# Performance work log

Measured on AMD Instinct MI355X. Metric: run time of the kernel, lower is better.

## Reference

```python
import jax, jax.numpy as jnp
import numpy as np
from jax import lax

VOCAB = 50000; EMB = 128; HID = 256; NL = 9; B = 128; T = 512; H = HID // 2; PAD = 0


def setup_inputs() -> dict:
    key = jax.random.key(0)
    ks = jax.random.split(key, 16)
    p = lambda k, s: jax.random.normal(k, s, jnp.float32) * 0.05
    return {
        "chars": jax.random.randint(ks[0], (B, T), 1, VOCAB),  # in [1, VOCAB) so mask fully on
        "labels": jax.random.randint(ks[1], (B, T), 0, NL),
        "emb": p(ks[2], (VOCAB, EMB)),
        "W_ih_f": p(ks[3], (4 * H, EMB)), "W_hh_f": p(ks[4], (4 * H, H)),
        "b_ih_f": p(ks[5], (4 * H,)), "b_hh_f": p(ks[6], (4 * H,)),
        "W_ih_b": p(ks[7], (4 * H, EMB)), "W_hh_b": p(ks[8], (4 * H, H)),
        "b_ih_b": p(ks[9], (4 * H,)), "b_hh_b": p(ks[10], (4 * H,)),
        "W_out": p(ks[11], (NL, HID)), "b_out": p(ks[12], (NL,)),
        "start_trans": p(ks[13], (NL,)), "end_trans": p(ks[14], (NL,)),
        "trans": p(ks[15], (NL, NL)),
    }


def _lstm(x, Wih, Whh, bih, bhh, reverse):
    # x: (B, T, D); PyTorch gate order i, f, g, o
    bsz = x.shape[0]
    h0 = jnp.zeros((bsz, H), x.dtype)
    c0 = jnp.zeros((bsz, H), x.dtype)
    b = bih + bhh

    def step(carry, xt):
        h, c = carry
        g = xt @ Wih.T + h @ Whh.T + b  # (B, 4H)
        i, f, gg, o = jnp.split(g, 4, axis=-1)
        c = jax.nn.sigmoid(f) * c + jax.nn.sigmoid(i) * jnp.tanh(gg)
        h = jax.nn.sigmoid(o) * jnp.tanh(c)
        return (h, c), h

    _, hs = lax.scan(step, (h0, c0), jnp.swapaxes(x, 0, 1), reverse=reverse)
    return jnp.swapaxes(hs, 0, 1)  # (B, T, H)


def _crf_nll(emissions, labels, mask, start, end, trans):
    # torchcrf linear-chain CRF log-likelihood, reduction='sum'
    maskf = mask.astype(emissions.dtype)
    emit = jnp.take_along_axis(emissions, labels[..., None], 2)[..., 0]  # (B, T)
    score = start[labels[:, 0]] + (emit * maskf).sum(1)
    score = score + (trans[labels[:, :-1], labels[:, 1:]] * maskf[:, 1:]).sum(1)
    last_idx = mask.sum(1).astype(jnp.int32) - 1
    last_tags = jnp.take_along_axis(labels, last_idx[:, None], 1)[:, 0]
    score = score + end[last_tags]

    # forward algorithm (log partition) as a scan over time
    alpha0 = start[None, :] + emissions[:, 0]  # (B, L)

    def step(alpha, inp):
        e_t, m_t = inp  # (B, L), (B,)
        nxt = jax.nn.logsumexp(alpha[:, :, None] + trans[None, :, :], axis=1) + e_t
        return jnp.where(m_t[:, None], nxt, alpha), None

    alpha, _ = lax.scan(step, alpha0,
                        (jnp.swapaxes(emissions, 0, 1)[1:], jnp.swapaxes(mask, 0, 1)[1:]))
    logZ = jax.nn.logsumexp(alpha + end[None, :], axis=-1)
    return -(score - logZ).sum()


def reference(chars, labels, emb, W_ih_f, W_hh_f, b_ih_f, b_hh_f,
              W_ih_b, W_hh_b, b_ih_b, b_hh_b, W_out, b_out,
              start_trans, end_trans, trans):
    x = emb[chars]  # (B, T, EMB)
    hf = _lstm(x, W_ih_f, W_hh_f, b_ih_f, b_hh_f, False)
    hb = _lstm(x, W_ih_b, W_hh_b, b_ih_b, b_hh_b, True)
    h = jnp.concatenate([hf, hb], axis=-1)  # (B, T, HID)
    emissions = h @ W_out.T + b_out  # dropout is identity in eval mode
    mask = chars != PAD
    return _crf_nll(emissions, labels, mask, start_trans, end_trans, trans)
```

## Files before the change

### kernel.cpp

```cpp
#include <hip/hip_runtime.h>

#define B_   128
#define T_   512
#define EMB_ 128
#define H_   128
#define NL_  9
#define MT_  65536

typedef __attribute__((ext_vector_type(8))) short short8v;
typedef __attribute__((ext_vector_type(4))) float float4v;

__device__ inline unsigned short f2bf(float f){
  unsigned u = __float_as_uint(f);
  u += 0x7FFFu + ((u >> 16) & 1u);
  return (unsigned short)(u >> 16);
}
__device__ inline float bf2f(unsigned short s){
  return __uint_as_float(((unsigned)s) << 16);
}

#define LOG2E 1.44269504f
__device__ inline float vexp2(float x){ float r; asm("v_exp_f32 %0, %1" : "=v"(r) : "v"(x)); return r; }
__device__ inline float vrcp (float x){ float r; asm("v_rcp_f32 %0, %1" : "=v"(r) : "v"(x)); return r; }

__device__ inline float lstm_cell(float pi, float pf, float pg, float po, float& c){
  float ei = vexp2(-LOG2E * pi);
  float ef = vexp2(-LOG2E * pf);
  float eg = vexp2( 2.f * LOG2E * pg);
  float eo = vexp2(-LOG2E * po);
  float R1 = vrcp((1.f + ei) * (1.f + eg));
  float ig = (eg - 1.f) * R1;
  float F  = vrcp(1.f + ef);
  c = fmaf(F, c, ig);
  float ec = vexp2(2.f * LOG2E * c);
  float R2 = vrcp((1.f + eo) * (1.f + ec));
  return (ec - 1.f) * R2;
}

__device__ inline void bar(){
  __builtin_amdgcn_sched_barrier(0);
  asm volatile("s_waitcnt lgkmcnt(0)" ::: "memory");
  __builtin_amdgcn_sched_barrier(0);
  __builtin_amdgcn_s_barrier();
  __builtin_amdgcn_sched_barrier(0);
}

__global__ void k0_prep(const float* __restrict__ Wihf, const float* __restrict__ Whhf,
                        const float* __restrict__ bihf, const float* __restrict__ bhhf,
                        const float* __restrict__ Wihb, const float* __restrict__ Whhb,
                        const float* __restrict__ bihb, const float* __restrict__ bhhb,
                        unsigned short* __restrict__ Wih2, unsigned short* __restrict__ Whh2,
                        float* __restrict__ biasc){
  int blk = blockIdx.x;
  int dir = blk >> 9;
  int nd  = blk & 511;
  int k   = threadIdx.x;
  int j = nd >> 2, g = nd & 3;
  int orig = g * 128 + j;
  const float* Wih = dir ? Wihb : Wihf;
  const float* Whh = dir ? Whhb : Whhf;
  Wih2[((long)(dir * 512 + nd)) * 128 + k] = f2bf(Wih[orig * EMB_ + k]);
  Whh2[((long)(dir * 512 + nd)) * 128 + k] = f2bf(Whh[orig * H_ + k]);
  if (k == 0){
    const float* bi = dir ? bihb : bihf;
    const float* bh = dir ? bhhb : bhhf;
    biasc[dir * 512 + nd] = bi[orig] + bh[orig];
  }
}

__global__ void k1_embed(const int* __restrict__ chars, const float* __restrict__ emb,
                         unsigned short* __restrict__ x){
  int i = blockIdx.x * blockDim.x + threadIdx.x;
  int m = i >> 5, q = i & 31;
  int c = chars[m];
  const float4* e4 = (const float4*)(emb + (long)c * EMB_);
  float4 v = e4[q];
  ushort4 o;
  o.x = f2bf(v.x); o.y = f2bf(v.y); o.z = f2bf(v.z); o.w = f2bf(v.w);
  *(ushort4*)(x + (long)m * EMB_ + q * 4) = o;
}

#define CST 130
__global__ __launch_bounds__(256) void k2_gemm(const unsigned short* __restrict__ x,
                                               const unsigned short* __restrict__ Wih2,
                                               const float* __restrict__ biasc,
                                               unsigned short* __restrict__ G){
  __shared__ unsigned short gsm[64 * CST];
  int w = threadIdx.x >> 6, lane = threadIdx.x & 63;
  int r = lane & 15, kb = (lane >> 4) * 8;
  long arow = (long)(blockIdx.x * 64 + w * 16 + r);
  short8v a[4];
  #pragma unroll
  for (int kf = 0; kf < 4; kf++)
    a[kf] = *(const short8v*)(x + arow * EMB_ + kf * 32 + kb);
  int ncol0 = blockIdx.y * 128;
  float4v acc[8];
  #pragma unroll
  for (int nf = 0; nf < 8; nf++){
    float4v z = {0.f, 0.f, 0.f, 0.f};
    acc[nf] = z;
    int wrow = ncol0 + nf * 16 + r;
    #pragma unroll
    for (int kf = 0; kf < 4; kf++){
      short8v bfrag = *(const short8v*)(Wih2 + (long)wrow * 128 + kf * 32 + kb);
      acc[nf] = __builtin_amdgcn_mfma_f32_16x16x32_bf16(a[kf], bfrag, acc[nf], 0, 0, 0);
    }
  }
  int rloc0 = w * 16 + (lane >> 4) * 4;
  #pragma unroll
  for (int nf = 0; nf < 8; nf++){
    int col = ncol0 + nf * 16 + r;
    float bia = biasc[col];
    #pragma unroll
    for (int reg = 0; reg < 4; reg++)
      gsm[(rloc0 + reg) * CST + nf * 16 + r] = f2bf(acc[nf][reg] + bia);
  }
  __syncthreads();
  #pragma unroll
  for (int it = 0; it < 4; it++){
    int u = it * 256 + threadIdx.x;
    int row = u >> 4, cu = u & 15;
    short8v v = *(const short8v*)&gsm[row * CST + cu * 8];
    *(short8v*)(G + (long)(blockIdx.x * 64 + row) * 1024 + ncol0 + cu * 8) = v;
  }
}

#define HBST 136
__global__ __launch_bounds__(1024, 1) void k3_scan4(
    const unsigned short* __restrict__ G,
    const unsigned short* __restrict__ Whh2,
    unsigned short* __restrict__ hs)
{
  const int blk = blockIdx.x;
  const int dir = blk >> 3;
  const int b0  = (blk & 7) * 16;
  const int tid = threadIdx.x;
  const int w   = tid >> 6;
  const int l   = tid & 63;
  const int r   = l & 15;
  const int q   = l >> 4;

  __shared__ unsigned short hR[8][16 * HBST];

  short8v Wf[2][4];
  #pragma unroll
  for (int t = 0; t < 2; t++){
    const unsigned short* wp = Whh2 + ((long)(dir * 512 + 32 * w + 16 * t + r)) * 128 + q * 8;
    #pragma unroll
    for (int kf = 0; kf < 4; kf++)
      Wf[t][kf] = *(const short8v*)(wp + kf * 32);
  }
  #pragma unroll
  for (int t = 0; t < 2; t++)
    #pragma unroll
    for (int kf = 0; kf < 4; kf++)
      asm volatile("" : "+v"(Wf[t][kf]));

  for (int i = tid; i < 16 * HBST; i += 1024) hR[7][i] = 0;

  float cc0 = 0.f, cc1 = 0.f;
  const int j0 = 8 * w + q;
  const int j1 = j0 + 4;
  const int fii = tid >> 8, fmm = (tid >> 4) & 15, fj8 = tid & 15;

  const long gstep = dir ? -1024L : 1024L;
  const unsigned short* gbase = G + ((long)(b0 + r) * T_ + (dir ? T_ - 1 : 0)) * 1024
                                  + dir * 512 + 32 * w + 4 * q;

#define ISSUEX(D0A, D0B, D1A, D1B, S) do{                          \
    const unsigned short* p_ = gbase + (long)(S) * gstep;          \
    D0A = *(const ushort4*)(p_);                                   \
    D0B = *(const ushort4*)(p_ + 16);                              \
    D1A = *(const ushort4*)(p_ + gstep);                           \
    D1B = *(const ushort4*)(p_ + gstep + 16);                      \
  }while(0)

#define STEPX(S, GA, GB) do{                                       \
    const int slot_r = ((S) + 7) & 7, slot_w = (S) & 7;            \
    const unsigned short* hrow = &hR[slot_r][r * HBST + q * 8];    \
    short8v hf0 = *(const short8v*)(hrow);                         \
    short8v hf1 = *(const short8v*)(hrow + 32);                    \
    short8v hf2 = *(const short8v*)(hrow + 64);                    \
    short8v hf3 = *(const short8v*)(hrow + 96);                    \
    float4v acc0 = {bf2f((GA).x), bf2f((GA).y), bf2f((GA).z), bf2f((GA).w)}; \
    float4v acc1 = {bf2f((GB).x), bf2f((GB).y), bf2f((GB).z), bf2f((GB).w)}; \
    acc0 = __builtin_amdgcn_mfma_f32_16x16x32_bf16(Wf[0][0], hf0, acc0, 0, 0, 0); \
    acc0 = __builtin_amdgcn_mfma_f32_16x16x32_bf16(Wf[0][1], hf1, acc0, 0, 0, 0); \
    acc0 = __builtin_amdgcn_mfma_f32_16x16x32_bf16(Wf[0][2], hf2, acc0, 0, 0, 0); \
    acc0 = __builtin_amdgcn_mfma_f32_16x16x32_bf16(Wf[0][3], hf3, acc0, 0, 0, 0); \
    acc1 = __builtin_amdgcn_mfma_f32_16x16x32_bf16(Wf[1][0], hf0, acc1, 0, 0, 0); \
    acc1 = __builtin_amdgcn_mfma_f32_16x16x32_bf16(Wf[1][1], hf1, acc1, 0, 0, 0); \
    acc1 = __builtin_amdgcn_mfma_f32_16x16x32_bf16(Wf[1][2], hf2, acc1, 0, 0, 0); \
    acc1 = __builtin_amdgcn_mfma_f32_16x16x32_bf16(Wf[1][3], hf3, acc1, 0, 0, 0); \
    float hv0 = lstm_cell(acc0[0], acc0[1], acc0[2], acc0[3], cc0);\
    float hv1 = lstm_cell(acc1[0], acc1[1], acc1[2], acc1[3], cc1);\
    unsigned pk_;                                                  \
    asm("v_cvt_pk_bf16_f32 %0, %1, %2" : "=v"(pk_) : "v"(hv0), "v"(hv1)); \
    unsigned short* wr = &hR[slot_w][r * HBST];                    \
    wr[j0] = (unsigned short)(pk_ & 0xffffu);                      \
    wr[j1] = (unsigned short)(pk_ >> 16);                          \
    bar();                                                         \
  }while(0)

#define FLUSHX(S4) do{                                             \
    int sg_ = (S4) - 4 + fii;                                      \
    int tg_ = dir ? (T_ - 1 - sg_) : sg_;                          \
    short8v v_ = *(const short8v*)&hR[sg_ & 7][fmm * HBST + fj8 * 8]; \
    *(short8v*)(hs + ((long)dir * MT_ + (long)(b0 + fmm) * T_ + tg_) * H_ + fj8 * 8) = v_; \
  }while(0)

  ushort4 A0a, A0b, A1a, A1b, B0a, B0b, B1a, B1b;
  ISSUEX(A0a, A0b, A1a, A1b, 0);
  bar();

  for (int s4 = 0; s4 < T_; s4 += 4){
    if (s4 > 0) FLUSHX(s4);
    ISSUEX(B0a, B0b, B1a, B1b, s4 + 2);
    STEPX(s4 + 0, A0a, A0b);
    STEPX(s4 + 1, A1a, A1b);
    if (s4 + 4 < T_) ISSUEX(A0a, A0b, A1a, A1b, s4 + 4);
    STEPX(s4 + 2, B0a, B0b);
    STEPX(s4 + 3, B1a, B1b);
  }
  FLUSHX(T_);

#undef ISSUEX
#undef STEPX
#undef FLUSHX
}

#define HSTR 264
__global__ __launch_bounds__(512) void k4_emis(const unsigned short* __restrict__ hs,
                                               const float* __restrict__ Wout,
                                               const float* __restrict__ bout,
                                               float* __restrict__ em){
  __shared__ float hcat[64 * HSTR];
  __shared__ float wo[NL_ * 256];
  int tid = threadIdx.x;
  int m0 = blockIdx.x * 64;
  const unsigned short* hf = hs;
  const unsigned short* hb = hs + (long)MT_ * H_;
  #pragma unroll
  for (int it = 0; it < 8; it++){
    int flat = it * 2048 + tid * 4;
    int r = flat >> 8, u = flat & 255;
    const unsigned short* src = (u < 128) ? (hf + (long)(m0 + r) * H_ + u)
                                          : (hb + (long)(m0 + r) * H_ + (u - 128));
    ushort4 v = *(const ushort4*)src;
    hcat[r * HSTR + u]     = bf2f(v.x);
    hcat[r * HSTR + u + 1] = bf2f(v.y);
    hcat[r * HSTR + u + 2] = bf2f(v.z);
    hcat[r * HSTR + u + 3] = bf2f(v.w);
  }
  for (int f = tid; f < NL_ * 256; f += 512) wo[f] = Wout[f];
  __syncthreads();
  #pragma unroll
  for (int half = 0; half < 2; half++){
    int idx = half * 512 + tid;
    if (idx < 64 * NL_){
      int r = idx / NL_, lbl = idx % NL_;
      float acc = bout[lbl];
      #pragma unroll 8
      for (int u = 0; u < 256; u++)
        acc = fmaf(hcat[r * HSTR + u], wo[lbl * 256 + u], acc);
      em[(long)(m0 + r) * NL_ + lbl] = acc;
    }
  }
}

__global__ void k5_crf(const float* __restrict__ em, const int* __restrict__ chars,
                       const int* __restrict__ labels, const float* __restrict__ startv,
                       const float* __restrict__ endv, const float* __restrict__ trans,
                       float* __restrict__ partial){
  int b = blockIdx.x, lane = threadIdx.x;
  const int* lab = labels + b * T_;
  const int* ch  = chars + b * T_;
  const float* e = em + (long)b * T_ * NL_;
  float sc = 0.f; int cnt = 0;
  for (int t = lane; t < T_; t += 64){
    int m = (ch[t] != 0);
    cnt += m;
    if (m){
      sc += e[t * NL_ + lab[t]];
      if (t > 0) sc += trans[lab[t - 1] * NL_ + lab[t]];
    }
  }
  #pragma unroll
  for (int off = 32; off; off >>= 1){
    sc  += __shfl_down(sc, off);
    cnt += __shfl_down(cnt, off);
  }
  sc  = __shfl(sc, 0);
  cnt = __shfl(cnt, 0);
  if (cnt < 1) cnt = 1;
  int jl = (lane < NL_) ? lane : 0;
  float tcol[NL_];
  #pragma unroll
  for (int i = 0; i < NL_; i++) tcol[i] = trans[i * NL_ + jl];
  float alpha = (lane < NL_) ? (startv[jl] + e[jl]) : -1e30f;
  float evn = (lane < NL_) ? e[NL_ + jl] : 0.f;
  int   mn  = (ch[1] != 0);
  for (int t = 1; t < T_; t++){
    float ev = evn; int m = mn;
    int t2 = (t + 1 < T_) ? t + 1 : t;
    evn = (lane < NL_) ? e[t2 * NL_ + jl] : 0.f;
    mn  = (ch[t2] != 0);
    float vv[NL_]; float mx = -1e30f;
    #pragma unroll
    for (int i = 0; i < NL_; i++){
      vv[i] = __shfl(alpha, i) + tcol[i];
      mx = fmaxf(mx, vv[i]);
    }
    float ssum = 0.f;
    #pragma unroll
    for (int i = 0; i < NL_; i++) ssum += __expf(vv[i] - mx);
    float nxt = mx + __logf(ssum) + ev;
    if (m && lane < NL_) alpha = nxt;
  }
  float av = (lane < NL_) ? (alpha + endv[jl]) : -1e30f;
  float mx = av;
  #pragma unroll
  for (int off = 8; off; off >>= 1) mx = fmaxf(mx, __shfl_down(mx, off));
  mx = __shfl(mx, 0);
  float ex = (lane < NL_) ? __expf(av - mx) : 0.f;
  #pragma unroll
  for (int off = 8; off; off >>= 1) ex += __shfl_down(ex, off);
  if (lane == 0){
    float logZ = mx + __logf(ex);
    float score = sc + startv[lab[0]] + endv[lab[cnt - 1]];
    partial[b] = logZ - score;
  }
}

__global__ void k6_reduce(const float* __restrict__ partial, float* __restrict__ out){
  int lane = threadIdx.x;
  float v = partial[lane];
  #pragma unroll
  for (int off = 32; off; off >>= 1) v += __shfl_down(v, off);
  __shared__ float tmp[2];
  if ((lane & 63) == 0) tmp[lane >> 6] = v;
  __syncthreads();
  if (lane == 0) out[0] = tmp[0] + tmp[1];
}

extern "C" void kernel_launch(void* const* d_in, const int* in_sizes, int n_in,
                              void* d_out, int out_size, void* d_ws, size_t ws_size,
                              hipStream_t stream){
  const int*   chars  = (const int*)d_in[0];
  const int*   labels = (const int*)d_in[1];
  const float* emb    = (const float*)d_in[2];
  const float* Wihf   = (const float*)d_in[3];
  const float* Whhf   = (const float*)d_in[4];
  const float* bihf   = (const float*)d_in[5];
  const float* bhhf   = (const float*)d_in[6];
  const float* Wihb   = (const float*)d_in[7];
  const float* Whhb   = (const float*)d_in[8];
  const float* bihb   = (const float*)d_in[9];
  const float* bhhb   = (const float*)d_in[10];
  const float* Wout   = (const float*)d_in[11];
  const float* bout   = (const float*)d_in[12];
  const float* startv = (const float*)d_in[13];
  const float* endv   = (const float*)d_in[14];
  const float* trans  = (const float*)d_in[15];

  char* ws = (char*)d_ws;
  unsigned short* x     = (unsigned short*)(ws);
  float*          em    = (float*)         (ws);
  float*          part  = (float*)         (ws + 2359296);
  unsigned short* Wih2  = (unsigned short*)(ws + 16777216);
  unsigned short* Whh2  = (unsigned short*)(ws + 17301504);
  float*          biasc = (float*)         (ws + 17825792);
  unsigned short* G     = (unsigned short*)(ws + 17829888);
  unsigned short* hs    = (unsigned short*)(ws + 152047616);

  hipLaunchKernelGGL(k0_prep,  dim3(1024), dim3(128), 0, stream,
                     Wihf, Whhf, bihf, bhhf, Wihb, Whhb, bihb, bhhb, Wih2, Whh2, biasc);
  hipLaunchKernelGGL(k1_embed, dim3(8192), dim3(256), 0, stream, chars, emb, x);
  hipLaunchKernelGGL(k2_gemm,  dim3(1024, 8), dim3(256), 0, stream, x, Wih2, biasc, G);
  hipLaunchKernelGGL(k3_scan4, dim3(16),   dim3(1024), 0, stream, G, Whh2, hs);
  hipLaunchKernelGGL(k4_emis,  dim3(1024), dim3(512), 0, stream, hs, Wout, bout, em);
  hipLaunchKernelGGL(k5_crf,   dim3(128),  dim3(64),  0, stream,
                     em, chars, labels, startv, endv, trans, part);
  hipLaunchKernelGGL(k6_reduce, dim3(1),   dim3(128), 0, stream, part, (float*)d_out);
}
```

Baseline: 963.0 us.

## Halve scan block to 8 waves, each computing four hidden-unit tiles per step

The recurrent LSTM scan kernel now runs 512 threads (8 waves) per block instead of 1024. Each wave holds four 16-row tiles of W_hh in registers and interleaves 16 MFMAs across four independent accumulators, so matrix latency is hidden within a wave. Fewer waves should make the per-timestep block barrier cheaper. The price is more VGPRs per wave, more serial cell math per wave, and a reworked prefetch and flush schedule.

```diff
diff --git a/kernel.cpp b/kernel.cpp
--- a/kernel.cpp
+++ b/kernel.cpp
@@ -126,7 +126,7 @@
 }
 
 #define HBST 136
-__global__ __launch_bounds__(1024, 1) void k3_scan4(
+__global__ __launch_bounds__(512, 1) void k3_scan5(
     const unsigned short* __restrict__ G,
     const unsigned short* __restrict__ Whh2,
     unsigned short* __restrict__ hs)
@@ -142,91 +142,104 @@
 
   __shared__ unsigned short hR[8][16 * HBST];
 
-  short8v Wf[2][4];
-  #pragma unroll
-  for (int t = 0; t < 2; t++){
-    const unsigned short* wp = Whh2 + ((long)(dir * 512 + 32 * w + 16 * t + r)) * 128 + q * 8;
+  short8v Wf[4][4];
+  #pragma unroll
+  for (int t = 0; t < 4; t++){
+    const unsigned short* wp = Whh2 + ((long)(dir * 512 + 64 * w + 16 * t + r)) * 128 + q * 8;
     #pragma unroll
     for (int kf = 0; kf < 4; kf++)
       Wf[t][kf] = *(const short8v*)(wp + kf * 32);
   }
   #pragma unroll
-  for (int t = 0; t < 2; t++)
+  for (int t = 0; t < 4; t++)
     #pragma unroll
     for (int kf = 0; kf < 4; kf++)
       asm volatile("" : "+v"(Wf[t][kf]));
 
-  for (int i = tid; i < 16 * HBST; i += 1024) hR[7][i] = 0;
-
-  float cc0 = 0.f, cc1 = 0.f;
-  const int j0 = 8 * w + q;
-  const int j1 = j0 + 4;
-  const int fii = tid >> 8, fmm = (tid >> 4) & 15, fj8 = tid & 15;
+  for (int i = tid; i < 16 * HBST; i += 512) hR[7][i] = 0;
+
+  float cc0 = 0.f, cc1 = 0.f, cc2 = 0.f, cc3 = 0.f;
+  const int jc0 = 16 * w + q;
 
   const long gstep = dir ? -1024L : 1024L;
   const unsigned short* gbase = G + ((long)(b0 + r) * T_ + (dir ? T_ - 1 : 0)) * 1024
-                                  + dir * 512 + 32 * w + 4 * q;
-
-#define ISSUEX(D0A, D0B, D1A, D1B, S) do{                          \
+                                  + dir * 512 + 64 * w + 4 * q;
+
+#define ISSUE5(D0, D1, D2, D3, S) do{                              \
     const unsigned short* p_ = gbase + (long)(S) * gstep;          \
-    D0A = *(const ushort4*)(p_);                                   \
-    D0B = *(const ushort4*)(p_ + 16);                              \
-    D1A = *(const ushort4*)(p_ + gstep);                           \
-    D1B = *(const ushort4*)(p_ + gstep + 16);                      \
+    D0 = *(const ushort4*)(p_);                                    \
+    D1 = *(const ushort4*)(p_ + 16);                               \
+    D2 = *(const ushort4*)(p_ + 32);                               \
+    D3 = *(const ushort4*)(p_ + 48);                               \
   }while(0)
 
-#define STEPX(S, GA, GB) do{                                       \
+#define STEP5(S, GA, GB, GC, GD) do{                               \
     const int slot_r = ((S) + 7) & 7, slot_w = (S) & 7;            \
     const unsigned short* hrow = &hR[slot_r][r * HBST + q * 8];    \
     short8v hf0 = *(const short8v*)(hrow);                         \
     short8v hf1 = *(const short8v*)(hrow + 32);                    \
     short8v hf2 = *(const short8v*)(hrow + 64);                    \
     short8v hf3 = *(const short8v*)(hrow + 96);                    \
-    float4v acc0 = {bf2f((GA).x), bf2f((GA).y), bf2f((GA).z), bf2f((GA).w)}; \
-    float4v acc1 = {bf2f((GB).x), bf2f((GB).y), bf2f((GB).z), bf2f((GB).w)}; \
-    acc0 = __builtin_amdgcn_mfma_f32_16x16x32_bf16(Wf[0][0], hf0, acc0, 0, 0, 0); \
-    acc0 = __builtin_amdgcn_mfma_f32_16x16x32_bf16(Wf[0][1], hf1, acc0, 0, 0, 0); \
-    acc0 = __builtin_amdgcn_mfma_f32_16x16x32_bf16(Wf[0][2], hf2, acc0, 0, 0, 0); \
-    acc0 = __builtin_amdgcn_mfma_f32_16x16x32_bf16(Wf[0][3], hf3, acc0, 0, 0, 0); \
-    acc1 = __builtin_amdgcn_mfma_f32_16x16x32_bf16(Wf[1][0], hf0, acc1, 0, 0, 0); \
-    acc1 = __builtin_amdgcn_mfma_f32_16x16x32_bf16(Wf[1][1], hf1, acc1, 0, 0, 0); \
-    acc1 = __builtin_amdgcn_mfma_f32_16x16x32_bf16(Wf[1][2], hf2, acc1, 0, 0, 0); \
-    acc1 = __builtin_amdgcn_mfma_f32_16x16x32_bf16(Wf[1][3], hf3, acc1, 0, 0, 0); \
-    float hv0 = lstm_cell(acc0[0], acc0[1], acc0[2], acc0[3], cc0);\
-    float hv1 = lstm_cell(acc1[0], acc1[1], acc1[2], acc1[3], cc1);\
-    unsigned pk_;                                                  \
-    asm("v_cvt_pk_bf16_f32 %0, %1, %2" : "=v"(pk_) : "v"(hv0), "v"(hv1)); \
-    unsigned short* wr = &hR[slot_w][r * HBST];                    \
-    wr[j0] = (unsigned short)(pk_ & 0xffffu);                      \
-    wr[j1] = (unsigned short)(pk_ >> 16);                          \
+    float4v a0 = {bf2f((GA).x), bf2f((GA).y), bf2f((GA).z), bf2f((GA).w)}; \
+    float4v a1 = {bf2f((GB).x), bf2f((GB).y), bf2f((GB).z), bf2f((GB).w)}; \
+    float4v a2 = {bf2f((GC).x), bf2f((GC).y), bf2f((GC).z), bf2f((GC).w)}; \
+    float4v a3 = {bf2f((GD).x), bf2f((GD).y), bf2f((GD).z), bf2f((GD).w)}; \
+    a0 = __builtin_amdgcn_mfma_f32_16x16x32_bf16(Wf[0][0], hf0, a0, 0, 0, 0);  \
+    a1 = __builtin_amdgcn_mfma_f32_16x16x32_bf16(Wf[1][0], hf0, a1, 0, 0, 0);  \
+    a2 = __builtin_amdgcn_mfma_f32_16x16x32_bf16(Wf[2][0], hf0, a2, 0, 0, 0);  \
+    a3 = __builtin_amdgcn_mfma_f32_16x16x32_bf16(Wf[3][0], hf0, a3, 0, 0, 0);  \
+    a0 = __builtin_amdgcn_mfma_f32_16x16x32_bf16(Wf[0][1], hf1, a0, 0, 0, 0);  \
+    a1 = __builtin_amdgcn_mfma_f32_16x16x32_bf16(Wf[1][1], hf1, a1, 0, 0, 0);  \
+    a2 = __builtin_amdgcn_mfma_f32_16x16x32_bf16(Wf[2][1], hf1, a2, 0, 0, 0);  \
+    a3 = __builtin_amdgcn_mfma_f32_16x16x32_bf16(Wf[3][1], hf1, a3, 0, 0, 0);  \
+    a0 = __builtin_amdgcn_mfma_f32_16x16x32_bf16(Wf[0][2], hf2, a0, 0, 0, 0);  \
+    a1 = __builtin_amdgcn_mfma_f32_16x16x32_bf16(Wf[1][2], hf2, a1, 0, 0, 0);  \
+    a2 = __builtin_amdgcn_mfma_f32_16x16x32_bf16(Wf[2][2], hf2, a2, 0, 0, 0);  \
+    a3 = __builtin_amdgcn_mfma_f32_16x16x32_bf16(Wf[3][2], hf2, a3, 0, 0, 0);  \
+    a0 = __builtin_amdgcn_mfma_f32_16x16x32_bf16(Wf[0][3], hf3, a0, 0, 0, 0);  \
+    a1 = __builtin_amdgcn_mfma_f32_16x16x32_bf16(Wf[1][3], hf3, a1, 0, 0, 0);  \
+    a2 = __builtin_amdgcn_mfma_f32_16x16x32_bf16(Wf[2][3], hf3, a2, 0, 0, 0);  \
+    a3 = __builtin_amdgcn_mfma_f32_16x16x32_bf16(Wf[3][3], hf3, a3, 0, 0, 0);  \
+    float hv0 = lstm_cell(a0[0], a0[1], a0[2], a0[3], cc0);        \
+    float hv1 = lstm_cell(a1[0], a1[1], a1[2], a1[3], cc1);        \
+    float hv2 = lstm_cell(a2[0], a2[1], a2[2], a2[3], cc2);        \
+    float hv3 = lstm_cell(a3[0], a3[1], a3[2], a3[3], cc3);        \
+    unsigned short* wr = &hR[slot_w][r * HBST + jc0];              \
+    wr[0]  = f2bf(hv0);                                            \
+    wr[4]  = f2bf(hv1);                                            \
+    wr[8]  = f2bf(hv2);                                            \
+    wr[12] = f2bf(hv3);                                            \
     bar();                                                         \
   }while(0)
 
-#define FLUSHX(S4) do{                                             \
-    int sg_ = (S4) - 4 + fii;                                      \
-    int tg_ = dir ? (T_ - 1 - sg_) : sg_;                          \
-    short8v v_ = *(const short8v*)&hR[sg_ & 7][fmm * HBST + fj8 * 8]; \
-    *(short8v*)(hs + ((long)dir * MT_ + (long)(b0 + fmm) * T_ + tg_) * H_ + fj8 * 8) = v_; \
+#define FLUSH5(S4) do{                                             \
+    _Pragma("unroll")                                              \
+    for (int it_ = 0; it_ < 2; it_++){                             \
+      int u_  = tid + it_ * 512;                                   \
+      int j8_ = u_ & 15, mm_ = (u_ >> 4) & 15, ii_ = u_ >> 8;      \
+      int sg_ = (S4) - 4 + ii_;                                    \
+      int tg_ = dir ? (T_ - 1 - sg_) : sg_;                        \
+      short8v v_ = *(const short8v*)&hR[sg_ & 7][mm_ * HBST + j8_ * 8]; \
+      *(short8v*)(hs + ((long)dir * MT_ + (long)(b0 + mm_) * T_ + tg_) * H_ + j8_ * 8) = v_; \
+    }                                                              \
   }while(0)
 
-  ushort4 A0a, A0b, A1a, A1b, B0a, B0b, B1a, B1b;
-  ISSUEX(A0a, A0b, A1a, A1b, 0);
+  ushort4 A0, A1, A2, A3, B0, B1, B2, B3;
+  ISSUE5(A0, A1, A2, A3, 0);
   bar();
 
-  for (int s4 = 0; s4 < T_; s4 += 4){
-    if (s4 > 0) FLUSHX(s4);
-    ISSUEX(B0a, B0b, B1a, B1b, s4 + 2);
-    STEPX(s4 + 0, A0a, A0b);
-    STEPX(s4 + 1, A1a, A1b);
-    if (s4 + 4 < T_) ISSUEX(A0a, A0b, A1a, A1b, s4 + 4);
-    STEPX(s4 + 2, B0a, B0b);
-    STEPX(s4 + 3, B1a, B1b);
-  }
-  FLUSHX(T_);
-
-#undef ISSUEX
-#undef STEPX
-#undef FLUSHX
+  for (int s4 = 0; s4 < T_; s4 += 2){
+    if ((s4 & 3) == 0 && s4 > 0) FLUSH5(s4);
+    if (s4 + 1 < T_) ISSUE5(B0, B1, B2, B3, s4 + 1);
+    STEP5(s4 + 0, A0, A1, A2, A3);
+    if (s4 + 2 < T_) ISSUE5(A0, A1, A2, A3, s4 + 2);
+    STEP5(s4 + 1, B0, B1, B2, B3);
+  }
+  FLUSH5(T_);
+
+#undef ISSUE5
+#undef STEP5
+#undef FLUSH5
 }
 
 #define HSTR 264
@@ -377,7 +390,7 @@
                      Wihf, Whhf, bihf, bhhf, Wihb, Whhb, bihb, bhhb, Wih2, Whh2, biasc);
   hipLaunchKernelGGL(k1_embed, dim3(8192), dim3(256), 0, stream, chars, emb, x);
   hipLaunchKernelGGL(k2_gemm,  dim3(1024, 8), dim3(256), 0, stream, x, Wih2, biasc, G);
-  hipLaunchKernelGGL(k3_scan4, dim3(16),   dim3(1024), 0, stream, G, Whh2, hs);
+  hipLaunchKernelGGL(k3_scan5, dim3(16),   dim3(512), 0, stream, G, Whh2, hs);
   hipLaunchKernelGGL(k4_emis,  dim3(1024), dim3(512), 0, stream, hs, Wout, bout, em);
   hipLaunchKernelGGL(k5_crf,   dim3(128),  dim3(64),  0, stream,
                      em, chars, labels, startv, endv, trans, part);
```

Measured after the change: 1.035 ms. 1.07x slower.
